# Kernel optimization log

Measured on AMD Instinct MI355X. Metric: run time of the kernel, lower is better.

The kernel has to match this reference:

```python
import jax, jax.numpy as jnp
import numpy as np

N_SRC, N_DST, DEG = 100000, 50000, 16
NODE_IN, EDGE_IN, HID = 128, 64, 64
E = N_DST * DEG


def sparsemax(z):
    # z: [..., K]; sparsemax along last axis (Martins & Astudillo)
    z = z - jnp.max(z, axis=-1, keepdims=True)
    zs = -jnp.sort(-z, axis=-1)  # descending sort
    k_range = jnp.arange(1, z.shape[-1] + 1, dtype=z.dtype)
    cs = jnp.cumsum(zs, axis=-1)
    is_gt = (1.0 + k_range * zs > cs).astype(z.dtype)
    k = jnp.max(is_gt * k_range, axis=-1, keepdims=True)
    tau = (jnp.sum(is_gt * zs, axis=-1, keepdims=True) - 1.0) / k
    return jnp.maximum(z - tau, 0.0)


def setup_inputs() -> dict:
    key = jax.random.key(0)
    ks = jax.random.split(key, 8)
    s = 0.02
    return {
        "node_features": jax.random.normal(ks[0], (N_SRC, NODE_IN), jnp.float32),
        "edge_features": jax.random.normal(ks[1], (E, EDGE_IN), jnp.float32),
        "src_idx": jax.random.randint(ks[2], (E,), 0, N_SRC, jnp.int32),
        "We": s * jax.random.normal(ks[3], (EDGE_IN, HID), jnp.float32),
        "be": jnp.zeros((HID,), jnp.float32),
        "Wa": s * jax.random.normal(ks[4], (EDGE_IN, HID), jnp.float32),
        "ba": jnp.zeros((HID,), jnp.float32),
        "wa": s * jax.random.normal(ks[5], (HID,), jnp.float32),
        "Wo": s * jax.random.normal(ks[6], (NODE_IN + HID, HID), jnp.float32),
        "bo": jnp.zeros((HID,), jnp.float32),
        "Wn": s * jax.random.normal(ks[7], (NODE_IN + HID, HID), jnp.float32),
        "bn": jnp.zeros((HID,), jnp.float32),
        "n_dst": N_DST,
        "deg": DEG,
    }


def reference(node_features, edge_features, src_idx, We, be, Wa, ba, wa, Wo, bo, Wn, bn, n_dst, deg):
    # dropout is identity in eval / p=0
    h_dst = node_features[:n_dst]                               # [n_dst, node_in]
    # message_func: per-edge transforms
    e_out = jax.nn.relu(edge_features @ We + be)                # [E, hid]
    a = jax.nn.leaky_relu((edge_features @ Wa + ba) @ wa)       # [E]
    h_src_e = node_features[src_idx]                            # gather [E, node_in]
    m = jax.nn.relu(jnp.concatenate([h_src_e, e_out], axis=-1) @ Wo + bo)  # [E, hid]
    # reduce_func: mailbox is [n_dst, deg, .] (fixed in-degree graph)
    a = a.reshape(n_dst, deg)
    m = m.reshape(n_dst, deg, -1)
    alpha = sparsemax(a)                                        # [n_dst, deg]
    h_neigh = jnp.einsum('nd,ndh->nh', alpha, m)                # [n_dst, hid]
    # node update
    return jax.nn.relu(jnp.concatenate([h_dst, h_neigh], axis=-1) @ Wn + bn)
```

## Files before the change

### kernel.cpp

```cpp
#include <hip/hip_runtime.h>


#define ND 50000

typedef __bf16 bf16x8 __attribute__((ext_vector_type(8)));
typedef float f32x16 __attribute__((ext_vector_type(16)));

__device__ __forceinline__ void sync_wave() {
  asm volatile("s_waitcnt lgkmcnt(0)" ::: "memory");
}

__device__ __forceinline__ unsigned short f2bf(float x) {
  unsigned u = __float_as_uint(x);
  u += 0x7fffu + ((u >> 16) & 1u);
  return (unsigned short)(u >> 16);
}

union Frag8 { bf16x8 v; unsigned u32[4]; };

__device__ __forceinline__ bf16x8 pack44(float4 a, float4 b) {
  Frag8 f;
  f.u32[0] = __builtin_amdgcn_perm(__float_as_uint(a.y) + 0x8000u,
                                   __float_as_uint(a.x) + 0x8000u, 0x07060302);
  f.u32[1] = __builtin_amdgcn_perm(__float_as_uint(a.w) + 0x8000u,
                                   __float_as_uint(a.z) + 0x8000u, 0x07060302);
  f.u32[2] = __builtin_amdgcn_perm(__float_as_uint(b.y) + 0x8000u,
                                   __float_as_uint(b.x) + 0x8000u, 0x07060302);
  f.u32[3] = __builtin_amdgcn_perm(__float_as_uint(b.w) + 0x8000u,
                                   __float_as_uint(b.z) + 0x8000u, 0x07060302);
  return f.v;
}

#define MFMA32(a, b, c) __builtin_amdgcn_mfma_f32_32x32x16_bf16((a), (b), (c), 0, 0, 0)

__device__ __forceinline__ f32x16 fzero16() {
  f32x16 c;
  #pragma unroll
  for (int r = 0; r < 16; ++r) c[r] = 0.f;
  return c;
}

extern "C" __global__ void __launch_bounds__(256, 2)
gteast_edge(const float* __restrict__ nf, const float* __restrict__ ef,
            const int* __restrict__ src,
            const float* __restrict__ Wa, const float* __restrict__ ba,
            const float* __restrict__ wa,
            const float* __restrict__ We, const float* __restrict__ be,
            const float* __restrict__ Wo, const float* __restrict__ bo,
            float* __restrict__ hn_out) {
  __shared__ unsigned short WoT[64 * 200];
  __shared__ unsigned short WeT[64 * 72];
  __shared__ unsigned short Et[4][32 * 72];
  __shared__ float vls[65];
  __shared__ float pr[260];

  const int tid = threadIdx.x;
  for (int i = tid; i < 64 * 64; i += 256) WeT[(i & 63) * 72 + (i >> 6)] = f2bf(We[i]);
  for (int i = tid; i < 192 * 64; i += 256) WoT[(i & 63) * 200 + (i >> 6)] = f2bf(Wo[i]);
  {
    const int k = tid >> 2, p = tid & 3;
    float s = 0.f;
    for (int h = 16 * p; h < 16 * p + 16; ++h) s += Wa[k * 64 + h] * wa[h];
    pr[tid] = s;
    if (tid < 4) {
      float sc = 0.f;
      for (int h = 16 * tid; h < 16 * tid + 16; ++h) sc += ba[h] * wa[h];
      pr[256 + tid] = sc;
    }
  }
  __syncthreads();
  if (tid < 64) vls[tid] = pr[4 * tid] + pr[4 * tid + 1] + pr[4 * tid + 2] + pr[4 * tid + 3];
  if (tid == 64) vls[64] = pr[256] + pr[257] + pr[258] + pr[259];
  __syncthreads();

  const int lane = tid & 63, w = tid >> 6;
  const int m = lane & 31, h8 = lane >> 5, t16 = lane & 15;
  const int wid = blockIdx.x * 4 + w;
  if (wid >= 3125) return;

  unsigned short* E = Et[w];
  const float cval = vls[64];
  float beL[2], boL[2];
  beL[0] = be[m]; beL[1] = be[32 + m];
  boL[0] = bo[m]; boL[1] = bo[32 + m];

  int s_cur = src[wid * 256 + m];

  #pragma unroll 2
  for (int it = 0; it < 8; ++it) {
    const int n0 = wid * 16 + it * 2;
    const long e0 = (long)wid * 256 + it * 32;

    const int s_nxt = (it < 7) ? src[e0 + 32 + m] : 0;

    const float* ep = ef + (e0 + m) * 64 + h8 * 8;
    float4 er[8];
    #pragma unroll
    for (int kc = 0; kc < 4; ++kc) {
      er[2 * kc] = *reinterpret_cast<const float4*>(ep + kc * 16);
      er[2 * kc + 1] = *reinterpret_cast<const float4*>(ep + kc * 16 + 4);
    }
    const float* hp = nf + (long)s_cur * 128 + h8 * 8;
    float4 nr[8];
    #pragma unroll
    for (int kc = 0; kc < 4; ++kc) {
      nr[2 * kc] = *reinterpret_cast<const float4*>(hp + kc * 16);
      nr[2 * kc + 1] = *reinterpret_cast<const float4*>(hp + kc * 16 + 4);
    }

    bf16x8 efF[4];
    float ap = 0.f;
    #pragma unroll
    for (int kc = 0; kc < 4; ++kc) {
      float4 a0 = er[2 * kc], a1 = er[2 * kc + 1];
      float4 v0 = *reinterpret_cast<const float4*>(&vls[kc * 16 + h8 * 8]);
      float4 v1 = *reinterpret_cast<const float4*>(&vls[kc * 16 + h8 * 8 + 4]);
      ap += a0.x * v0.x + a0.y * v0.y + a0.z * v0.z + a0.w * v0.w;
      ap += a1.x * v1.x + a1.y * v1.y + a1.z * v1.z + a1.w * v1.w;
      efF[kc] = pack44(a0, a1);
    }
    ap += __shfl_xor(ap, 32);
    float a = ap + cval;
    a = a > 0.f ? a : 0.01f * a;

    #pragma unroll
    for (int nt = 0; nt < 2; ++nt) {
      f32x16 c = fzero16();
      #pragma unroll
      for (int kc = 0; kc < 4; ++kc)
        c = MFMA32(efF[kc],
                   *reinterpret_cast<const bf16x8*>(&WeT[(nt * 32 + m) * 72 + kc * 16 + h8 * 8]), c);
      #pragma unroll
      for (int r = 0; r < 16; ++r) {
        const int row = (r & 3) + 8 * (r >> 2) + 4 * h8;
        E[row * 72 + nt * 32 + m] = f2bf(fmaxf(c[r] + beL[nt], 0.f));
      }
    }
    sync_wave();

    float4 nr2[8];
    #pragma unroll
    for (int kc = 0; kc < 4; ++kc) {
      nr2[2 * kc] = *reinterpret_cast<const float4*>(hp + 64 + kc * 16);
      nr2[2 * kc + 1] = *reinterpret_cast<const float4*>(hp + 64 + kc * 16 + 4);
    }

    f32x16 cM0 = fzero16(), cM1 = fzero16();
    #pragma unroll
    for (int kc = 0; kc < 12; ++kc) {
      bf16x8 af;
      if (kc < 4) af = pack44(nr[2 * kc], nr[2 * kc + 1]);
      else if (kc < 8) af = pack44(nr2[2 * (kc - 4)], nr2[2 * (kc - 4) + 1]);
      else af = *reinterpret_cast<const bf16x8*>(&E[m * 72 + (kc - 8) * 16 + h8 * 8]);
      cM0 = MFMA32(af, *reinterpret_cast<const bf16x8*>(&WoT[m * 200 + kc * 16 + h8 * 8]), cM0);
      cM1 = MFMA32(af, *reinterpret_cast<const bf16x8*>(&WoT[(32 + m) * 200 + kc * 16 + h8 * 8]), cM1);
    }
    sync_wave();
    #pragma unroll
    for (int r = 0; r < 16; ++r) {
      cM0[r] = fmaxf(cM0[r] + boL[0], 0.f);
      cM1[r] = fmaxf(cM1[r] + boL[1], 0.f);
    }

    float z = a;
    #pragma unroll
    for (int k = 2; k <= 16; k <<= 1) {
      #pragma unroll
      for (int j = k >> 1; j > 0; j >>= 1) {
        float o = __shfl_xor(z, j);
        const bool upper = (t16 & j) != 0;
        const bool desc = (t16 & k) == 0;
        z = (upper != desc) ? fmaxf(z, o) : fminf(z, o);
      }
    }
    float cs = z;
    #pragma unroll
    for (int off = 1; off < 16; off <<= 1) {
      float o = __shfl_up(cs, off, 16);
      cs += (t16 >= off) ? o : 0.f;
    }
    const bool gt = 1.f + (float)(t16 + 1) * z > cs;
    float kf = gt ? (float)(t16 + 1) : 0.f;
    float sv = gt ? z : 0.f;
    #pragma unroll
    for (int mm = 1; mm < 16; mm <<= 1) {
      kf = fmaxf(kf, __shfl_xor(kf, mm));
      sv += __shfl_xor(sv, mm);
    }
    const float tau = (sv - 1.f) / kf;
    const float alpha = fmaxf(a - tau, 0.f);

    float al[16];
    #pragma unroll
    for (int r = 0; r < 16; ++r)
      al[r] = __shfl(alpha, (r & 3) + 8 * (r >> 2) + 4 * h8);
    float p00 = 0.f, p01 = 0.f, p10 = 0.f, p11 = 0.f;
    #pragma unroll
    for (int r = 0; r < 8; ++r) {
      p00 += al[r] * cM0[r];      p01 += al[r] * cM1[r];
      p10 += al[8 + r] * cM0[8 + r]; p11 += al[8 + r] * cM1[8 + r];
    }
    p00 += __shfl_xor(p00, 32); p01 += __shfl_xor(p01, 32);
    p10 += __shfl_xor(p10, 32); p11 += __shfl_xor(p11, 32);
    const float v0 = h8 ? p10 : p00;
    const float v1 = h8 ? p11 : p01;
    hn_out[(long)(n0 + h8) * 64 + m] = v0;
    hn_out[(long)(n0 + h8) * 64 + 32 + m] = v1;

    s_cur = s_nxt;
  }
}

extern "C" __global__ void __launch_bounds__(256, 2)
gteast_out(const float* __restrict__ nf, const float* __restrict__ Wn,
           const float* __restrict__ bn, float* __restrict__ out) {
  __shared__ unsigned short WnT[64 * 200];
  const int tid = threadIdx.x;
  for (int i = tid; i < 192 * 64; i += 256) WnT[(i & 63) * 200 + (i >> 6)] = f2bf(Wn[i]);
  __syncthreads();

  const int lane = tid & 63, w = tid >> 6;
  const int m = lane & 31, h8 = lane >> 5;
  const int tile = blockIdx.x * 4 + w;
  if (tile >= 1563) return;
  const int r0 = tile * 32;

  float bnL[2];
  bnL[0] = bn[m]; bnL[1] = bn[32 + m];

  const float* hp = nf + (long)(r0 + m) * 128 + h8 * 8;
  const int hr = min(r0 + m, ND - 1);
  const float* gp = out + (long)hr * 64 + h8 * 8;

  float4 nr[8], nr2[8], gr[8];
  #pragma unroll
  for (int kc = 0; kc < 4; ++kc) {
    nr[2 * kc] = *reinterpret_cast<const float4*>(hp + kc * 16);
    nr[2 * kc + 1] = *reinterpret_cast<const float4*>(hp + kc * 16 + 4);
  }
  #pragma unroll
  for (int kc = 0; kc < 4; ++kc) {
    nr2[2 * kc] = *reinterpret_cast<const float4*>(hp + 64 + kc * 16);
    nr2[2 * kc + 1] = *reinterpret_cast<const float4*>(hp + 64 + kc * 16 + 4);
  }
  #pragma unroll
  for (int kc = 0; kc < 4; ++kc) {
    gr[2 * kc] = *reinterpret_cast<const float4*>(gp + kc * 16);
    gr[2 * kc + 1] = *reinterpret_cast<const float4*>(gp + kc * 16 + 4);
  }

  f32x16 c0 = fzero16(), c1 = fzero16();
  #pragma unroll
  for (int kc = 0; kc < 12; ++kc) {
    bf16x8 af;
    if (kc < 4) af = pack44(nr[2 * kc], nr[2 * kc + 1]);
    else if (kc < 8) af = pack44(nr2[2 * (kc - 4)], nr2[2 * (kc - 4) + 1]);
    else af = pack44(gr[2 * (kc - 8)], gr[2 * (kc - 8) + 1]);
    c0 = MFMA32(af, *reinterpret_cast<const bf16x8*>(&WnT[m * 200 + kc * 16 + h8 * 8]), c0);
    c1 = MFMA32(af, *reinterpret_cast<const bf16x8*>(&WnT[(32 + m) * 200 + kc * 16 + h8 * 8]), c1);
  }

  #pragma unroll
  for (int r = 0; r < 16; ++r) {
    const int row = (r & 3) + 8 * (r >> 2) + 4 * h8;
    const int grow = r0 + row;
    if (grow < ND) {
      out[(long)grow * 64 + m] = fmaxf(c0[r] + bnL[0], 0.f);
      out[(long)grow * 64 + 32 + m] = fmaxf(c1[r] + bnL[1], 0.f);
    }
  }
}

extern "C" void kernel_launch(void* const* d_in, const int* in_sizes, int n_in,
                              void* d_out, int out_size, void* d_ws, size_t ws_size,
                              hipStream_t stream) {
  const float* nf = (const float*)d_in[0];
  const float* ef = (const float*)d_in[1];
  const int* si   = (const int*)d_in[2];
  const float* We = (const float*)d_in[3];
  const float* be = (const float*)d_in[4];
  const float* Wa = (const float*)d_in[5];
  const float* ba = (const float*)d_in[6];
  const float* wa = (const float*)d_in[7];
  const float* Wo = (const float*)d_in[8];
  const float* bo = (const float*)d_in[9];
  const float* Wn = (const float*)d_in[10];
  const float* bn = (const float*)d_in[11];
  float* out = (float*)d_out;

  gteast_edge<<<782, 256, 0, stream>>>(nf, ef, si, Wa, ba, wa, We, be, Wo, bo, out);
  gteast_out<<<391, 256, 0, stream>>>(nf, Wn, bn, out);
}
```

Measured before the change: 421.6 us.

## Software-pipeline edge and gather loads across iterations and raise occupancy

```diff
diff --git a/kernel.cpp b/kernel.cpp
--- a/kernel.cpp
+++ b/kernel.cpp
@@ -40,7 +40,7 @@
   return c;
 }
 
-extern "C" __global__ void __launch_bounds__(256, 2)
+extern "C" __global__ void __launch_bounds__(256, 3)
 gteast_edge(const float* __restrict__ nf, const float* __restrict__ ef,
             const int* __restrict__ src,
             const float* __restrict__ Wa, const float* __restrict__ ba,
@@ -50,11 +50,12 @@
             float* __restrict__ hn_out) {
   __shared__ unsigned short WoT[64 * 200];
   __shared__ unsigned short WeT[64 * 72];
-  __shared__ unsigned short Et[4][32 * 72];
-  __shared__ float vls[65];
-  __shared__ float pr[260];
+  __shared__ __align__(16) unsigned short Et[4][32 * 72];
+  __shared__ float vls[68];
 
   const int tid = threadIdx.x;
+  float* pr = reinterpret_cast<float*>(&Et[0][0]);
+
   for (int i = tid; i < 64 * 64; i += 256) WeT[(i & 63) * 72 + (i >> 6)] = f2bf(We[i]);
   for (int i = tid; i < 192 * 64; i += 256) WoT[(i & 63) * 200 + (i >> 6)] = f2bf(Wo[i]);
   {
@@ -85,27 +86,36 @@
   boL[0] = bo[m]; boL[1] = bo[32 + m];
 
   int s_cur = src[wid * 256 + m];
-
-  #pragma unroll 2
+  float4 er[8], nr1[8];
+  {
+    const float* ep = ef + ((long)wid * 256 + m) * 64 + h8 * 8;
+    #pragma unroll
+    for (int kc = 0; kc < 4; ++kc) {
+      er[2 * kc] = *reinterpret_cast<const float4*>(ep + kc * 16);
+      er[2 * kc + 1] = *reinterpret_cast<const float4*>(ep + kc * 16 + 4);
+    }
+    const float* hp = nf + (long)s_cur * 128 + h8 * 8;
+    #pragma unroll
+    for (int kc = 0; kc < 4; ++kc) {
+      nr1[2 * kc] = *reinterpret_cast<const float4*>(hp + kc * 16);
+      nr1[2 * kc + 1] = *reinterpret_cast<const float4*>(hp + kc * 16 + 4);
+    }
+  }
+
+  #pragma unroll 1
   for (int it = 0; it < 8; ++it) {
     const int n0 = wid * 16 + it * 2;
     const long e0 = (long)wid * 256 + it * 32;
 
-    const int s_nxt = (it < 7) ? src[e0 + 32 + m] : 0;
-
-    const float* ep = ef + (e0 + m) * 64 + h8 * 8;
-    float4 er[8];
-    #pragma unroll
-    for (int kc = 0; kc < 4; ++kc) {
-      er[2 * kc] = *reinterpret_cast<const float4*>(ep + kc * 16);
-      er[2 * kc + 1] = *reinterpret_cast<const float4*>(ep + kc * 16 + 4);
-    }
-    const float* hp = nf + (long)s_cur * 128 + h8 * 8;
-    float4 nr[8];
-    #pragma unroll
-    for (int kc = 0; kc < 4; ++kc) {
-      nr[2 * kc] = *reinterpret_cast<const float4*>(hp + kc * 16);
-      nr[2 * kc + 1] = *reinterpret_cast<const float4*>(hp + kc * 16 + 4);
+    const int s_nxt = (it < 7) ? src[e0 + 32 + m] : s_cur;
+    float4 nr2[8];
+    {
+      const float* hp2 = nf + (long)s_cur * 128 + h8 * 8 + 64;
+      #pragma unroll
+      for (int kc = 0; kc < 4; ++kc) {
+        nr2[2 * kc] = *reinterpret_cast<const float4*>(hp2 + kc * 16);
+        nr2[2 * kc + 1] = *reinterpret_cast<const float4*>(hp2 + kc * 16 + 4);
+      }
     }
 
     bf16x8 efF[4];
@@ -138,22 +148,34 @@
     }
     sync_wave();
 
-    float4 nr2[8];
-    #pragma unroll
-    for (int kc = 0; kc < 4; ++kc) {
-      nr2[2 * kc] = *reinterpret_cast<const float4*>(hp + 64 + kc * 16);
-      nr2[2 * kc + 1] = *reinterpret_cast<const float4*>(hp + 64 + kc * 16 + 4);
-    }
+    bf16x8 af[8];
+    #pragma unroll
+    for (int kc = 0; kc < 4; ++kc) af[kc] = pack44(nr1[2 * kc], nr1[2 * kc + 1]);
+    {
+      const long eoff = e0 + (it < 7 ? 32 : 0);
+      const float* ep = ef + (eoff + m) * 64 + h8 * 8;
+      #pragma unroll
+      for (int kc = 0; kc < 4; ++kc) {
+        er[2 * kc] = *reinterpret_cast<const float4*>(ep + kc * 16);
+        er[2 * kc + 1] = *reinterpret_cast<const float4*>(ep + kc * 16 + 4);
+      }
+      const float* hp = nf + (long)s_nxt * 128 + h8 * 8;
+      #pragma unroll
+      for (int kc = 0; kc < 4; ++kc) {
+        nr1[2 * kc] = *reinterpret_cast<const float4*>(hp + kc * 16);
+        nr1[2 * kc + 1] = *reinterpret_cast<const float4*>(hp + kc * 16 + 4);
+      }
+    }
+    #pragma unroll
+    for (int kc = 0; kc < 4; ++kc) af[4 + kc] = pack44(nr2[2 * kc], nr2[2 * kc + 1]);
 
     f32x16 cM0 = fzero16(), cM1 = fzero16();
     #pragma unroll
     for (int kc = 0; kc < 12; ++kc) {
-      bf16x8 af;
-      if (kc < 4) af = pack44(nr[2 * kc], nr[2 * kc + 1]);
-      else if (kc < 8) af = pack44(nr2[2 * (kc - 4)], nr2[2 * (kc - 4) + 1]);
-      else af = *reinterpret_cast<const bf16x8*>(&E[m * 72 + (kc - 8) * 16 + h8 * 8]);
-      cM0 = MFMA32(af, *reinterpret_cast<const bf16x8*>(&WoT[m * 200 + kc * 16 + h8 * 8]), cM0);
-      cM1 = MFMA32(af, *reinterpret_cast<const bf16x8*>(&WoT[(32 + m) * 200 + kc * 16 + h8 * 8]), cM1);
+      bf16x8 afc = (kc < 8) ? af[kc]
+                            : *reinterpret_cast<const bf16x8*>(&E[m * 72 + (kc - 8) * 16 + h8 * 8]);
+      cM0 = MFMA32(afc, *reinterpret_cast<const bf16x8*>(&WoT[m * 200 + kc * 16 + h8 * 8]), cM0);
+      cM1 = MFMA32(afc, *reinterpret_cast<const bf16x8*>(&WoT[(32 + m) * 200 + kc * 16 + h8 * 8]), cM1);
     }
     sync_wave();
     #pragma unroll
@@ -197,21 +219,19 @@
     float p00 = 0.f, p01 = 0.f, p10 = 0.f, p11 = 0.f;
     #pragma unroll
     for (int r = 0; r < 8; ++r) {
-      p00 += al[r] * cM0[r];      p01 += al[r] * cM1[r];
-      p10 += al[8 + r] * cM0[8 + r]; p11 += al[8 + r] * cM1[8 + r];
+      p00 += al[r] * cM0[r];          p01 += al[r] * cM1[r];
+      p10 += al[8 + r] * cM0[8 + r];  p11 += al[8 + r] * cM1[8 + r];
     }
     p00 += __shfl_xor(p00, 32); p01 += __shfl_xor(p01, 32);
     p10 += __shfl_xor(p10, 32); p11 += __shfl_xor(p11, 32);
-    const float v0 = h8 ? p10 : p00;
-    const float v1 = h8 ? p11 : p01;
-    hn_out[(long)(n0 + h8) * 64 + m] = v0;
-    hn_out[(long)(n0 + h8) * 64 + 32 + m] = v1;
+    hn_out[(long)(n0 + h8) * 64 + m] = h8 ? p10 : p00;
+    hn_out[(long)(n0 + h8) * 64 + 32 + m] = h8 ? p11 : p01;
 
     s_cur = s_nxt;
   }
 }
 
-extern "C" __global__ void __launch_bounds__(256, 2)
+extern "C" __global__ void __launch_bounds__(256, 4)
 gteast_out(const float* __restrict__ nf, const float* __restrict__ Wn,
            const float* __restrict__ bn, float* __restrict__ out) {
   __shared__ unsigned short WnT[64 * 200];
```

After: 439.2 us. 1.04x slower.
